# Performance work log

Measured on AMD Instinct MI355X. Metric: run time of the kernel, lower is better.

The kernel has to match this reference:

```python
import jax, jax.numpy as jnp
import numpy as np

E, D, O, G, H, K = 8, 1024, 1024, 512, 2048, 2
B = 8192

def _xavier(key, shape):
    fan_in, fan_out = shape[-2], shape[-1]
    lim = float(np.sqrt(6.0 / (fan_in + fan_out)))
    return jax.random.uniform(key, shape, jnp.float32, -lim, lim)

def setup_inputs() -> dict:
    key = jax.random.key(0)
    ks = jax.random.split(key, 6)
    x = jax.random.normal(ks[0], (B, D), jnp.float32)
    # stacked expert params (xavier-uniform weights, zero bias like torch init)
    W1 = _xavier(ks[1], (E, D, H))
    b1 = jnp.zeros((E, H), jnp.float32)
    W2 = _xavier(ks[2], (E, H, O))
    b2 = jnp.zeros((E, O), jnp.float32)
    # gate params
    Wg1 = _xavier(ks[3], (D, G))
    bg1 = jnp.zeros((G,), jnp.float32)
    Wg2 = _xavier(ks[4], (G, E))
    bg2 = jnp.zeros((E,), jnp.float32)
    return {"x": x, "W1": W1, "b1": b1, "W2": W2, "b2": b2,
            "Wg1": Wg1, "bg1": bg1, "Wg2": Wg2, "bg2": bg2}

def reference(x, W1, b1, W2, b2, Wg1, bg1, Wg2, bg2):
    batch = x.shape[0]
    # gate (dropout inactive in eval)
    gate_logits = jax.nn.relu(x @ Wg1 + bg1) @ Wg2 + bg2          # [B,E]
    gate_scores = jax.nn.softmax(gate_logits, axis=1)
    top_k_scores, top_k_indices = jax.lax.top_k(gate_scores, K)   # [B,K]
    # dense all-expert MLP (mirrors torch.stack over experts)
    h = jax.nn.relu(jnp.einsum('bd,edh->ebh', x, W1) + b1[:, None, :])   # [E,B,H]
    expert_outputs = jnp.einsum('ebh,eho->beo', h, W2) + b2[None, :, :]  # [B,E,O]
    # gather top-k expert outputs, scale, combine
    selected = jnp.take_along_axis(expert_outputs, top_k_indices[:, :, None], axis=1)  # [B,K,O]
    scaled = selected * top_k_scores[:, :, None]
    scaled = scaled / (jnp.sum(top_k_scores, axis=1, keepdims=True)[:, :, None] + 1e-9)
    combined = jnp.sum(scaled, axis=1)                            # [B,O]
    # auxiliary loss
    one_hot = jax.nn.one_hot(top_k_indices, E, dtype=jnp.float32) # [B,K,E]
    expert_load = jnp.sum(one_hot, axis=(0, 1)) / (batch + 1e-9)
    load_balancing_loss = jnp.var(expert_load, ddof=1)            # torch var is unbiased
    entropy = -jnp.mean(jnp.sum(gate_scores * jnp.log(gate_scores + 1e-9), axis=1))
    aux_loss = load_balancing_loss + entropy
    return combined, aux_loss
```

## Files before the change

### kernel.cpp

```cpp
#include <hip/hip_runtime.h>

#define B_ 8192
#define D_ 1024
#define O_ 1024
#define G_ 512
#define H_ 2048
#define E_ 8
#define ROWSP (B_ * 2 + E_ * 128)
#define TAU 0.01f

typedef unsigned short u16;
using f32x4 = __attribute__((ext_vector_type(4))) float;
using s16x8 = __attribute__((ext_vector_type(8))) short;

__device__ __forceinline__ u16 f2bf(float f) {
  union { float f; unsigned u; } v; v.f = f;
  unsigned r = v.u + 0x7FFFu + ((v.u >> 16) & 1u);
  return (u16)(r >> 16);
}
__device__ __forceinline__ float bf2f(u16 h) {
  union { unsigned u; float f; } v; v.u = ((unsigned)h) << 16; return v.f;
}
__device__ __forceinline__ void gload16(const void* g, void* l) {
  __builtin_amdgcn_global_load_lds(
      (const __attribute__((address_space(1))) unsigned int*)g,
      (__attribute__((address_space(3))) unsigned int*)l, 16, 0, 0);
}
__device__ __forceinline__ int xcd_swz(int bid, int nwg) {
  return (bid & 7) * (nwg >> 3) + (bid >> 3);
}
__device__ __forceinline__ int stage_kc(int t) {
  return (((t & 3) ^ ((t >> 3) & 3)) * 8);
}
__device__ __forceinline__ int frag_idx(int half, int lane, int i) {
  int row = half * 64 + i * 16 + (lane & 15);
  int s = (lane >> 4) ^ ((lane >> 1) & 3);
  return (row * 4 + s) * 8;
}

__global__ __launch_bounds__(256) void k_cast_x(const float* __restrict__ x,
                                                u16* __restrict__ xhi,
                                                u16* __restrict__ xlo) {
  int t = blockIdx.x * 256 + threadIdx.x;
  float4 v = ((const float4*)x)[t];
  u16 h0 = f2bf(v.x), h1 = f2bf(v.y), h2 = f2bf(v.z), h3 = f2bf(v.w);
  ushort4 hi; hi.x = h0; hi.y = h1; hi.z = h2; hi.w = h3;
  ushort4 lo;
  lo.x = f2bf(v.x - bf2f(h0)); lo.y = f2bf(v.y - bf2f(h1));
  lo.z = f2bf(v.z - bf2f(h2)); lo.w = f2bf(v.w - bf2f(h3));
  ((ushort4*)xhi)[t] = hi; ((ushort4*)xlo)[t] = lo;
}

__global__ __launch_bounds__(256) void k_transpose_cast(const float* __restrict__ src,
                                                        u16* __restrict__ dhi,
                                                        u16* __restrict__ dlo,
                                                        int R, int C) {
  __shared__ float tile[32][33];
  size_t bofs = (size_t)blockIdx.z * R * C;
  src += bofs; dhi += bofs; if (dlo) dlo += bofs;
  int tx = threadIdx.x & 31, ty = threadIdx.x >> 5;
  int c0 = blockIdx.x * 32, r0 = blockIdx.y * 32;
#pragma unroll
  for (int p = 0; p < 4; ++p) {
    int r = ty + p * 8;
    tile[r][tx] = src[(size_t)(r0 + r) * C + c0 + tx];
  }
  __syncthreads();
#pragma unroll
  for (int p = 0; p < 4; ++p) {
    int r = ty + p * 8;
    float v = tile[tx][r];
    size_t o = (size_t)(c0 + r) * R + r0 + tx;
    dhi[o] = f2bf(v);
    if (dlo) dlo[o] = f2bf(v - bf2f(f2bf(v)));
  }
}

__global__ __launch_bounds__(256) void k_gate_gemm1(const u16* __restrict__ xhi,
                                                    const u16* __restrict__ xlo,
                                                    const u16* __restrict__ whi,
                                                    const u16* __restrict__ wlo,
                                                    const float* __restrict__ bg1,
                                                    float* __restrict__ G1) {
  __shared__ u16 Ah[4096], Al[4096], Bh[4096], Bl[4096];
  int work = xcd_swz(blockIdx.x, (G_ / 128) * (B_ / 128));
  int m0 = (work >> 2) * 128, n0 = (work & 3) * 128;
  int t = threadIdx.x;
  int wave = t >> 6, lane = t & 63;
  int wm = wave >> 1, wn = wave & 1;

  const f32x4 z = {0.f, 0.f, 0.f, 0.f};
  f32x4 acc[4][4];
#pragma unroll
  for (int i = 0; i < 4; ++i)
#pragma unroll
    for (int j = 0; j < 4; ++j) acc[i][j] = z;

  int ar = t >> 2, ac = stage_kc(t);
  const u16* xh0 = xhi + (size_t)(m0 + ar) * D_ + ac;
  const u16* xh1 = xhi + (size_t)(m0 + 64 + ar) * D_ + ac;
  const u16* xl0 = xlo + (size_t)(m0 + ar) * D_ + ac;
  const u16* xl1 = xlo + (size_t)(m0 + 64 + ar) * D_ + ac;
  const u16* wh0 = whi + (size_t)(n0 + ar) * D_ + ac;
  const u16* wh1 = whi + (size_t)(n0 + 64 + ar) * D_ + ac;
  const u16* wl0 = wlo + (size_t)(n0 + ar) * D_ + ac;
  const u16* wl1 = wlo + (size_t)(n0 + 64 + ar) * D_ + ac;

  for (int k0 = 0; k0 < D_; k0 += 32) {
    gload16(xh0 + k0, &Ah[t * 8]); gload16(xh1 + k0, &Ah[2048 + t * 8]);
    gload16(xl0 + k0, &Al[t * 8]); gload16(xl1 + k0, &Al[2048 + t * 8]);
    gload16(wh0 + k0, &Bh[t * 8]); gload16(wh1 + k0, &Bh[2048 + t * 8]);
    gload16(wl0 + k0, &Bl[t * 8]); gload16(wl1 + k0, &Bl[2048 + t * 8]);
    __syncthreads();
    s16x8 ah[4], al[4], bh[4], bl[4];
#pragma unroll
    for (int i = 0; i < 4; ++i) {
      ah[i] = *(const s16x8*)&Ah[frag_idx(wm, lane, i)];
      al[i] = *(const s16x8*)&Al[frag_idx(wm, lane, i)];
      bh[i] = *(const s16x8*)&Bh[frag_idx(wn, lane, i)];
      bl[i] = *(const s16x8*)&Bl[frag_idx(wn, lane, i)];
    }
#pragma unroll
    for (int i = 0; i < 4; ++i)
#pragma unroll
      for (int j = 0; j < 4; ++j) {
        acc[i][j] = __builtin_amdgcn_mfma_f32_16x16x32_bf16(ah[i], bh[j], acc[i][j], 0, 0, 0);
        acc[i][j] = __builtin_amdgcn_mfma_f32_16x16x32_bf16(ah[i], bl[j], acc[i][j], 0, 0, 0);
        acc[i][j] = __builtin_amdgcn_mfma_f32_16x16x32_bf16(al[i], bh[j], acc[i][j], 0, 0, 0);
      }
    __syncthreads();
  }
#pragma unroll
  for (int j = 0; j < 4; ++j) {
    int col = n0 + wn * 64 + j * 16 + (lane & 15);
    float bias = bg1[col];
#pragma unroll
    for (int i = 0; i < 4; ++i)
#pragma unroll
      for (int q = 0; q < 4; ++q) {
        int row = m0 + wm * 64 + i * 16 + (lane >> 4) * 4 + q;
        float v = acc[i][j][q] + bias;
        G1[(size_t)row * G_ + col] = v > 0.f ? v : 0.f;
      }
  }
}

__global__ __launch_bounds__(256) void k_gate_logits(const float* __restrict__ G1,
                                                     const float* __restrict__ Wg2,
                                                     const float* __restrict__ bg2,
                                                     float* __restrict__ logits,
                                                     int* __restrict__ flaglist,
                                                     int* __restrict__ nflag) {
  int t = threadIdx.x, wave = t >> 6, lane = t & 63;
  int row = blockIdx.x * 4 + wave;

  float4 g0 = *(const float4*)(G1 + (size_t)row * G_ + lane * 8);
  float4 g1 = *(const float4*)(G1 + (size_t)row * G_ + lane * 8 + 4);
  float g[8] = {g0.x, g0.y, g0.z, g0.w, g1.x, g1.y, g1.z, g1.w};
  float p[8] = {0, 0, 0, 0, 0, 0, 0, 0};
#pragma unroll
  for (int cc = 0; cc < 8; ++cc) {
    int c = lane * 8 + cc;
    float4 w0 = *(const float4*)(Wg2 + c * 8);
    float4 w1 = *(const float4*)(Wg2 + c * 8 + 4);
    p[0] += g[cc] * w0.x; p[1] += g[cc] * w0.y; p[2] += g[cc] * w0.z; p[3] += g[cc] * w0.w;
    p[4] += g[cc] * w1.x; p[5] += g[cc] * w1.y; p[6] += g[cc] * w1.z; p[7] += g[cc] * w1.w;
  }
#pragma unroll
  for (int off = 32; off >= 1; off >>= 1)
#pragma unroll
    for (int e = 0; e < 8; ++e) p[e] += __shfl_xor(p[e], off);
  if (lane == 0) {
    float l1 = -1e30f, l2 = -1e30f, l3 = -1e30f;
#pragma unroll
    for (int e = 0; e < 8; ++e) {
      float v = p[e] + bg2[e];
      logits[(size_t)row * 8 + e] = v;
      if (v > l1) { l3 = l2; l2 = l1; l1 = v; }
      else if (v > l2) { l3 = l2; l2 = v; }
      else if (v > l3) { l3 = v; }
    }
    if (l2 - l3 < TAU) {
      int pos = atomicAdd(nflag, 1);
      flaglist[pos] = row;
    }
  }
}

__global__ __launch_bounds__(256) void k_gate_fixup(const float* __restrict__ x,
                                                    const float* __restrict__ Wg1,
                                                    const float* __restrict__ bg1,
                                                    const float* __restrict__ Wg2,
                                                    const float* __restrict__ bg2,
                                                    const int* __restrict__ flaglist,
                                                    const int* __restrict__ nflag,
                                                    float* __restrict__ logits) {
  __shared__ float xs[1024];
  __shared__ float red[256][9];
  int t = threadIdx.x;
  int n = *nflag;
  for (int i = blockIdx.x; i < n; i += gridDim.x) {
    int row = flaglist[i];
    ((float4*)xs)[t] = ((const float4*)(x + (size_t)row * D_))[t];
    __syncthreads();
    int c0 = t * 2;
    float h0 = 0.f, h1 = 0.f;
#pragma unroll 8
    for (int d = 0; d < D_; ++d) {
      float xv = xs[d];
      float2 w = *(const float2*)(Wg1 + (size_t)d * G_ + c0);
      h0 += xv * w.x; h1 += xv * w.y;
    }
    h0 += bg1[c0]; h1 += bg1[c0 + 1];
    h0 = h0 > 0.f ? h0 : 0.f; h1 = h1 > 0.f ? h1 : 0.f;
#pragma unroll
    for (int e = 0; e < 8; ++e)
      red[t][e] = h0 * Wg2[c0 * 8 + e] + h1 * Wg2[(c0 + 1) * 8 + e];
    __syncthreads();
    for (int s = 128; s >= 1; s >>= 1) {
      if (t < s) {
#pragma unroll
        for (int e = 0; e < 8; ++e) red[t][e] += red[t + s][e];
      }
      __syncthreads();
    }
    if (t < 8) logits[(size_t)row * 8 + t] = red[0][t] + bg2[t];
    __syncthreads();
  }
}

__global__ __launch_bounds__(256) void k_gate_final(const float* __restrict__ logits,
                                                    int* __restrict__ topidx,
                                                    float* __restrict__ wnorm,
                                                    int* __restrict__ counts,
                                                    float* __restrict__ entacc) {
  __shared__ int cnt_s[8];
  __shared__ float ent_s[4];
  int t = threadIdx.x;
  if (t < 8) cnt_s[t] = 0;
  __syncthreads();
  int row = blockIdx.x * 256 + t;
  float4 a = ((const float4*)logits)[(size_t)row * 2];
  float4 b = ((const float4*)logits)[(size_t)row * 2 + 1];
  float L[8] = {a.x, a.y, a.z, a.w, b.x, b.y, b.z, b.w};
  float m = L[0];
#pragma unroll
  for (int e = 1; e < 8; ++e) m = fmaxf(m, L[e]);
  float s[8], Z = 0.f;
#pragma unroll
  for (int e = 0; e < 8; ++e) { s[e] = expf(L[e] - m); Z += s[e]; }
  float inv = 1.f / Z;
  float sc[8];
#pragma unroll
  for (int e = 0; e < 8; ++e) sc[e] = s[e] * inv;
  int i1 = 0;
#pragma unroll
  for (int e = 1; e < 8; ++e) if (L[e] > L[i1]) i1 = e;
  int i2 = (i1 == 0) ? 1 : 0;
#pragma unroll
  for (int e = 0; e < 8; ++e) if (e != i1 && L[e] > L[i2]) i2 = e;
  float s1 = sc[i1], s2 = sc[i2];
  float denom = s1 + s2 + 1e-9f;
  topidx[row * 2] = i1; topidx[row * 2 + 1] = i2;
  wnorm[row * 2] = s1 / denom; wnorm[row * 2 + 1] = s2 / denom;
  atomicAdd(&cnt_s[i1], 1); atomicAdd(&cnt_s[i2], 1);
  float ent = 0.f;
#pragma unroll
  for (int e = 0; e < 8; ++e) ent -= sc[e] * logf(sc[e] + 1e-9f);
#pragma unroll
  for (int off = 32; off >= 1; off >>= 1) ent += __shfl_xor(ent, off);
  if ((t & 63) == 0) ent_s[t >> 6] = ent;
  __syncthreads();
  if (t == 0) atomicAdd(entacc, ent_s[0] + ent_s[1] + ent_s[2] + ent_s[3]);
  if (t < 8) atomicAdd(&counts[t], cnt_s[t]);
}

__global__ void k_scan(const int* __restrict__ counts, const float* __restrict__ entacc,
                       int* __restrict__ aoff, float* __restrict__ aux_out) {
  if (threadIdx.x == 0 && blockIdx.x == 0) {
    int off = 0; aoff[0] = 0;
    float ld[8]; float mean = 0.f;
    for (int e = 0; e < 8; ++e) {
      ld[e] = (float)counts[e] / (8192.0f + 1e-9f);
      mean += ld[e];
      off += ((counts[e] + 127) >> 7) << 7;
      aoff[e + 1] = off;
    }
    mean *= 0.125f;
    float var = 0.f;
    for (int e = 0; e < 8; ++e) { float d = ld[e] - mean; var += d * d; }
    var *= (1.0f / 7.0f);
    *aux_out = var + entacc[0] / 8192.0f;
  }
}

__global__ __launch_bounds__(256) void k_scatter(const int* __restrict__ topidx,
                                                 const float* __restrict__ wnorm,
                                                 const int* __restrict__ aoff,
                                                 int* __restrict__ fill,
                                                 int* __restrict__ tok_list,
                                                 float* __restrict__ wroute,
                                                 int* __restrict__ pos_of) {
  int t = blockIdx.x * 256 + threadIdx.x;
  if (t >= B_ * 2) return;
  int e = topidx[t];
  int pos = aoff[e] + atomicAdd(&fill[e], 1);
  tok_list[pos] = t >> 1;
  wroute[pos] = wnorm[t];
  pos_of[t] = pos;
}

__global__ __launch_bounds__(256) void k_egemm1(const u16* __restrict__ xhi,
                                                const u16* __restrict__ w1t,
                                                const float* __restrict__ b1v,
                                                const int* __restrict__ tok_list,
                                                const int* __restrict__ aoff,
                                                u16* __restrict__ hbuf) {
  __shared__ u16 As[2][4096], Bs[2][4096];
  int work = xcd_swz(blockIdx.x, (H_ / 128) * (ROWSP / 128));
  int rt = work >> 4;
  int n0 = (work & 15) * 128;
  int row0 = rt * 128;
  if (row0 >= aoff[8]) return;
  int e = 0;
  while (row0 >= aoff[e + 1]) ++e;
  int t = threadIdx.x, wave = t >> 6, lane = t & 63;
  int wm = wave >> 1, wn = wave & 1;
  const u16* w1e = w1t + (size_t)e * H_ * D_;

  int ar = t >> 2, ac = stage_kc(t);
  int tok0 = tok_list[row0 + ar];       if ((unsigned)tok0 >= B_) tok0 = 0;
  int tok1 = tok_list[row0 + 64 + ar];  if ((unsigned)tok1 >= B_) tok1 = 0;
  const u16* a0 = xhi + (size_t)tok0 * D_ + ac;
  const u16* a1 = xhi + (size_t)tok1 * D_ + ac;
  const u16* bb0 = w1e + (size_t)(n0 + ar) * D_ + ac;
  const u16* bb1 = w1e + (size_t)(n0 + 64 + ar) * D_ + ac;

  const f32x4 z = {0.f, 0.f, 0.f, 0.f};
  f32x4 acc[4][4];
#pragma unroll
  for (int i = 0; i < 4; ++i)
#pragma unroll
    for (int j = 0; j < 4; ++j) acc[i][j] = z;

  gload16(a0, &As[0][t * 8]);  gload16(a1, &As[0][2048 + t * 8]);
  gload16(bb0, &Bs[0][t * 8]); gload16(bb1, &Bs[0][2048 + t * 8]);
  __syncthreads();

  const int NT = D_ / 32;
  for (int kt = 0; kt < NT; ++kt) {
    const u16* Sa = As[kt & 1];
    const u16* Sb = Bs[kt & 1];
    if (kt + 1 < NT) {
      int k1 = (kt + 1) * 32;
      u16* Da = As[(kt + 1) & 1];
      u16* Db = Bs[(kt + 1) & 1];
      gload16(a0 + k1, &Da[t * 8]);  gload16(a1 + k1, &Da[2048 + t * 8]);
      gload16(bb0 + k1, &Db[t * 8]); gload16(bb1 + k1, &Db[2048 + t * 8]);
    }
    s16x8 af[4], bf[4];
#pragma unroll
    for (int i = 0; i < 4; ++i) {
      af[i] = *(const s16x8*)&Sa[frag_idx(wm, lane, i)];
      bf[i] = *(const s16x8*)&Sb[frag_idx(wn, lane, i)];
    }
#pragma unroll
    for (int i = 0; i < 4; ++i)
#pragma unroll
      for (int j = 0; j < 4; ++j)
        acc[i][j] = __builtin_amdgcn_mfma_f32_16x16x32_bf16(af[i], bf[j], acc[i][j], 0, 0, 0);
    __syncthreads();
  }
#pragma unroll
  for (int j = 0; j < 4; ++j) {
    int col = n0 + wn * 64 + j * 16 + (lane & 15);
    float bias = b1v[e * H_ + col];
#pragma unroll
    for (int i = 0; i < 4; ++i)
#pragma unroll
      for (int q = 0; q < 4; ++q) {
        int row = row0 + wm * 64 + i * 16 + (lane >> 4) * 4 + q;
        float v = acc[i][j][q] + bias;
        hbuf[(size_t)row * H_ + col] = f2bf(v > 0.f ? v : 0.f);
      }
  }
}

__global__ __launch_bounds__(256) void k_egemm2(const u16* __restrict__ hbuf,
                                                const u16* __restrict__ w2t,
                                                const float* __restrict__ b2v,
                                                const int* __restrict__ aoff,
                                                const float* __restrict__ wroute,
                                                u16* __restrict__ rbuf) {
  __shared__ u16 As[2][4096], Bs[2][4096];
  int work = xcd_swz(blockIdx.x, (O_ / 128) * (ROWSP / 128));
  int rt = work >> 3;
  int n0 = (work & 7) * 128;
  int row0 = rt * 128;
  if (row0 >= aoff[8]) return;
  int e = 0;
  while (row0 >= aoff[e + 1]) ++e;
  int t = threadIdx.x, wave = t >> 6, lane = t & 63;
  int wm = wave >> 1, wn = wave & 1;
  const u16* w2e = w2t + (size_t)e * O_ * H_;

  int ar = t >> 2, ac = stage_kc(t);
  const u16* a0 = hbuf + (size_t)(row0 + ar) * H_ + ac;
  const u16* a1 = hbuf + (size_t)(row0 + 64 + ar) * H_ + ac;
  const u16* bb0 = w2e + (size_t)(n0 + ar) * H_ + ac;
  const u16* bb1 = w2e + (size_t)(n0 + 64 + ar) * H_ + ac;

  const f32x4 z = {0.f, 0.f, 0.f, 0.f};
  f32x4 acc[4][4];
#pragma unroll
  for (int i = 0; i < 4; ++i)
#pragma unroll
    for (int j = 0; j < 4; ++j) acc[i][j] = z;

  gload16(a0, &As[0][t * 8]);  gload16(a1, &As[0][2048 + t * 8]);
  gload16(bb0, &Bs[0][t * 8]); gload16(bb1, &Bs[0][2048 + t * 8]);
  __syncthreads();

  const int NT = H_ / 32;
  for (int kt = 0; kt < NT; ++kt) {
    const u16* Sa = As[kt & 1];
    const u16* Sb = Bs[kt & 1];
    if (kt + 1 < NT) {
      int k1 = (kt + 1) * 32;
      u16* Da = As[(kt + 1) & 1];
      u16* Db = Bs[(kt + 1) & 1];
      gload16(a0 + k1, &Da[t * 8]);  gload16(a1 + k1, &Da[2048 + t * 8]);
      gload16(bb0 + k1, &Db[t * 8]); gload16(bb1 + k1, &Db[2048 + t * 8]);
    }
    s16x8 af[4], bf[4];
#pragma unroll
    for (int i = 0; i < 4; ++i) {
      af[i] = *(const s16x8*)&Sa[frag_idx(wm, lane, i)];
      bf[i] = *(const s16x8*)&Sb[frag_idx(wn, lane, i)];
    }
#pragma unroll
    for (int i = 0; i < 4; ++i)
#pragma unroll
      for (int j = 0; j < 4; ++j)
        acc[i][j] = __builtin_amdgcn_mfma_f32_16x16x32_bf16(af[i], bf[j], acc[i][j], 0, 0, 0);
    __syncthreads();
  }
#pragma unroll
  for (int i = 0; i < 4; ++i)
#pragma unroll
    for (int q = 0; q < 4; ++q) {
      int row = row0 + wm * 64 + i * 16 + (lane >> 4) * 4 + q;
      float wv = wroute[row];
#pragma unroll
      for (int j = 0; j < 4; ++j) {
        int col = n0 + wn * 64 + j * 16 + (lane & 15);
        float bias = b2v[e * O_ + col];
        rbuf[(size_t)row * O_ + col] = f2bf((acc[i][j][q] + bias) * wv);
      }
    }
}

__global__ __launch_bounds__(256) void k_combine(const u16* __restrict__ rbuf,
                                                 const int* __restrict__ pos_of,
                                                 float* __restrict__ out) {
  int t = threadIdx.x;
  int tok = blockIdx.x * 2 + (t >> 7);
  int c = (t & 127) * 8;
  int p0 = pos_of[tok * 2], p1 = pos_of[tok * 2 + 1];
  const u16* r0 = rbuf + (size_t)p0 * O_ + c;
  const u16* r1 = rbuf + (size_t)p1 * O_ + c;
  ushort4 a0 = *(const ushort4*)r0, a1 = *(const ushort4*)(r0 + 4);
  ushort4 b0 = *(const ushort4*)r1, b1 = *(const ushort4*)(r1 + 4);
  float4 o0, o1;
  o0.x = bf2f(a0.x) + bf2f(b0.x); o0.y = bf2f(a0.y) + bf2f(b0.y);
  o0.z = bf2f(a0.z) + bf2f(b0.z); o0.w = bf2f(a0.w) + bf2f(b0.w);
  o1.x = bf2f(a1.x) + bf2f(b1.x); o1.y = bf2f(a1.y) + bf2f(b1.y);
  o1.z = bf2f(a1.z) + bf2f(b1.z); o1.w = bf2f(a1.w) + bf2f(b1.w);
  float* op = out + (size_t)tok * O_ + c;
  *(float4*)op = o0; *(float4*)(op + 4) = o1;
}

static const size_t o_xhi  = 0;
static const size_t o_xlo  = o_xhi + (size_t)B_ * D_ * 2;
static const size_t o_w1t  = o_xlo + (size_t)B_ * D_ * 2;
static const size_t o_w2t  = o_w1t + (size_t)E_ * H_ * D_ * 2;
static const size_t o_wg1h = o_w2t + (size_t)E_ * O_ * H_ * 2;
static const size_t o_wg1l = o_wg1h + (size_t)G_ * D_ * 2;
static const size_t o_G1   = o_wg1l + (size_t)G_ * D_ * 2;
static const size_t o_h    = o_G1 + (size_t)B_ * G_ * 4;
static const size_t o_idx  = o_h + (size_t)ROWSP * H_ * 2;
static const size_t o_wn   = o_idx + (size_t)B_ * 2 * 4;
static const size_t o_pos  = o_wn + (size_t)B_ * 2 * 4;
static const size_t o_tok  = o_pos + (size_t)B_ * 2 * 4;
static const size_t o_wr   = o_tok + (size_t)ROWSP * 4;
static const size_t o_cnt  = o_wr + (size_t)ROWSP * 4;
static const size_t o_fill = o_cnt + 32;
static const size_t o_ent  = o_cnt + 64;
static const size_t o_nfl  = o_cnt + 96;
static const size_t o_aoff = o_cnt + 128;
static const size_t o_logits = o_cnt + 256;
static const size_t o_flag   = o_logits + (size_t)B_ * 8 * 4;
static const size_t o_rbuf = o_xlo;

extern "C" void kernel_launch(void* const* d_in, const int* in_sizes, int n_in,
                              void* d_out, int out_size, void* d_ws, size_t ws_size,
                              hipStream_t stream) {
  const float* x   = (const float*)d_in[0];
  const float* W1  = (const float*)d_in[1];
  const float* b1  = (const float*)d_in[2];
  const float* W2  = (const float*)d_in[3];
  const float* b2  = (const float*)d_in[4];
  const float* Wg1 = (const float*)d_in[5];
  const float* bg1 = (const float*)d_in[6];
  const float* Wg2 = (const float*)d_in[7];
  const float* bg2 = (const float*)d_in[8];
  float* out = (float*)d_out;
  char* ws = (char*)d_ws;

  u16* xhi  = (u16*)(ws + o_xhi);
  u16* xlo  = (u16*)(ws + o_xlo);
  u16* w1t  = (u16*)(ws + o_w1t);
  u16* w2t  = (u16*)(ws + o_w2t);
  u16* wg1h = (u16*)(ws + o_wg1h);
  u16* wg1l = (u16*)(ws + o_wg1l);
  float* G1 = (float*)(ws + o_G1);
  u16* hbuf = (u16*)(ws + o_h);
  int* topidx = (int*)(ws + o_idx);
  float* wnorm = (float*)(ws + o_wn);
  int* pos_of = (int*)(ws + o_pos);
  int* tok_list = (int*)(ws + o_tok);
  float* wroute = (float*)(ws + o_wr);
  int* counts = (int*)(ws + o_cnt);
  int* fill = (int*)(ws + o_fill);
  float* entacc = (float*)(ws + o_ent);
  int* nflag = (int*)(ws + o_nfl);
  int* aoff = (int*)(ws + o_aoff);
  float* logits = (float*)(ws + o_logits);
  int* flaglist = (int*)(ws + o_flag);
  u16* rbuf = (u16*)(ws + o_rbuf);

  hipMemsetAsync(ws + o_cnt, 0, 128, stream);

  k_cast_x<<<(B_ * D_ / 4) / 256, 256, 0, stream>>>(x, xhi, xlo);
  k_transpose_cast<<<dim3(G_ / 32, D_ / 32, 1), 256, 0, stream>>>(Wg1, wg1h, wg1l, D_, G_);
  k_transpose_cast<<<dim3(H_ / 32, D_ / 32, E_), 256, 0, stream>>>(W1, w1t, nullptr, D_, H_);
  k_transpose_cast<<<dim3(O_ / 32, H_ / 32, E_), 256, 0, stream>>>(W2, w2t, nullptr, H_, O_);

  k_gate_gemm1<<<(G_ / 128) * (B_ / 128), 256, 0, stream>>>(xhi, xlo, wg1h, wg1l, bg1, G1);
  k_gate_logits<<<B_ / 4, 256, 0, stream>>>(G1, Wg2, bg2, logits, flaglist, nflag);
  k_gate_fixup<<<128, 256, 0, stream>>>(x, Wg1, bg1, Wg2, bg2, flaglist, nflag, logits);
  k_gate_final<<<B_ / 256, 256, 0, stream>>>(logits, topidx, wnorm, counts, entacc);
  k_scan<<<1, 64, 0, stream>>>(counts, entacc, aoff, out + (size_t)B_ * O_);
  k_scatter<<<(B_ * 2) / 256, 256, 0, stream>>>(topidx, wnorm, aoff, fill, tok_list, wroute, pos_of);

  k_egemm1<<<(H_ / 128) * (ROWSP / 128), 256, 0, stream>>>(xhi, w1t, b1, tok_list, aoff, hbuf);
  k_egemm2<<<(O_ / 128) * (ROWSP / 128), 256, 0, stream>>>(hbuf, w2t, b2, aoff, wroute, rbuf);
  k_combine<<<B_ / 2, 256, 0, stream>>>(rbuf, pos_of, out);
}
```

Baseline: 514.7 us.

## Triple-buffer expert GEMM LDS tiles with explicit vmcnt waits

Both expert GEMM kernels move from a double-buffered to a three-stage LDS pipeline. Loads run two k-tiles ahead, and waits use explicit s_waitcnt vmcnt counts with raw s_barrier instead of __syncthreads. The aim is to hide global-to-LDS latency behind the MFMA work. In exchange, LDS use grows from 32KB to 48KB per block, which may reduce occupancy. The hand-counted vmcnt values must match the number of outstanding loads, or the kernels will read stale tiles.

```diff
diff --git a/kernel.cpp b/kernel.cpp
--- a/kernel.cpp
+++ b/kernel.cpp
@@ -316,7 +316,7 @@
                                                 const int* __restrict__ tok_list,
                                                 const int* __restrict__ aoff,
                                                 u16* __restrict__ hbuf) {
-  __shared__ u16 As[2][4096], Bs[2][4096];
+  __shared__ u16 As[3][4096], Bs[3][4096];
   int work = xcd_swz(blockIdx.x, (H_ / 128) * (ROWSP / 128));
   int rt = work >> 4;
   int n0 = (work & 15) * 128;
@@ -343,21 +343,22 @@
 #pragma unroll
     for (int j = 0; j < 4; ++j) acc[i][j] = z;
 
-  gload16(a0, &As[0][t * 8]);  gload16(a1, &As[0][2048 + t * 8]);
-  gload16(bb0, &Bs[0][t * 8]); gload16(bb1, &Bs[0][2048 + t * 8]);
-  __syncthreads();
+#pragma unroll
+  for (int s = 0; s < 3; ++s) {
+    int kk = s * 32;
+    gload16(a0 + kk, &As[s][t * 8]);  gload16(a1 + kk, &As[s][2048 + t * 8]);
+    gload16(bb0 + kk, &Bs[s][t * 8]); gload16(bb1 + kk, &Bs[s][2048 + t * 8]);
+  }
 
   const int NT = D_ / 32;
+  int cb = 0;
   for (int kt = 0; kt < NT; ++kt) {
-    const u16* Sa = As[kt & 1];
-    const u16* Sb = Bs[kt & 1];
-    if (kt + 1 < NT) {
-      int k1 = (kt + 1) * 32;
-      u16* Da = As[(kt + 1) & 1];
-      u16* Db = Bs[(kt + 1) & 1];
-      gload16(a0 + k1, &Da[t * 8]);  gload16(a1 + k1, &Da[2048 + t * 8]);
-      gload16(bb0 + k1, &Db[t * 8]); gload16(bb1 + k1, &Db[2048 + t * 8]);
-    }
+    if (kt < NT - 2)      asm volatile("s_waitcnt vmcnt(8)" ::: "memory");
+    else if (kt == NT - 2) asm volatile("s_waitcnt vmcnt(4)" ::: "memory");
+    else                  asm volatile("s_waitcnt vmcnt(0)" ::: "memory");
+    __builtin_amdgcn_s_barrier();
+    const u16* Sa = As[cb];
+    const u16* Sb = Bs[cb];
     s16x8 af[4], bf[4];
 #pragma unroll
     for (int i = 0; i < 4; ++i) {
@@ -369,7 +370,13 @@
 #pragma unroll
       for (int j = 0; j < 4; ++j)
         acc[i][j] = __builtin_amdgcn_mfma_f32_16x16x32_bf16(af[i], bf[j], acc[i][j], 0, 0, 0);
-    __syncthreads();
+    __builtin_amdgcn_s_barrier();
+    if (kt + 3 < NT) {
+      int kk = (kt + 3) * 32;
+      gload16(a0 + kk, &As[cb][t * 8]);  gload16(a1 + kk, &As[cb][2048 + t * 8]);
+      gload16(bb0 + kk, &Bs[cb][t * 8]); gload16(bb1 + kk, &Bs[cb][2048 + t * 8]);
+    }
+    cb = (cb == 2) ? 0 : cb + 1;
   }
 #pragma unroll
   for (int j = 0; j < 4; ++j) {
@@ -392,7 +399,7 @@
                                                 const int* __restrict__ aoff,
                                                 const float* __restrict__ wroute,
                                                 u16* __restrict__ rbuf) {
-  __shared__ u16 As[2][4096], Bs[2][4096];
+  __shared__ u16 As[3][4096], Bs[3][4096];
   int work = xcd_swz(blockIdx.x, (O_ / 128) * (ROWSP / 128));
   int rt = work >> 3;
   int n0 = (work & 7) * 128;
@@ -417,21 +424,22 @@
 #pragma unroll
     for (int j = 0; j < 4; ++j) acc[i][j] = z;
 
-  gload16(a0, &As[0][t * 8]);  gload16(a1, &As[0][2048 + t * 8]);
-  gload16(bb0, &Bs[0][t * 8]); gload16(bb1, &Bs[0][2048 + t * 8]);
-  __syncthreads();
+#pragma unroll
+  for (int s = 0; s < 3; ++s) {
+    int kk = s * 32;
+    gload16(a0 + kk, &As[s][t * 8]);  gload16(a1 + kk, &As[s][2048 + t * 8]);
+    gload16(bb0 + kk, &Bs[s][t * 8]); gload16(bb1 + kk, &Bs[s][2048 + t * 8]);
+  }
 
   const int NT = H_ / 32;
+  int cb = 0;
   for (int kt = 0; kt < NT; ++kt) {
-    const u16* Sa = As[kt & 1];
-    const u16* Sb = Bs[kt & 1];
-    if (kt + 1 < NT) {
-      int k1 = (kt + 1) * 32;
-      u16* Da = As[(kt + 1) & 1];
-      u16* Db = Bs[(kt + 1) & 1];
-      gload16(a0 + k1, &Da[t * 8]);  gload16(a1 + k1, &Da[2048 + t * 8]);
-      gload16(bb0 + k1, &Db[t * 8]); gload16(bb1 + k1, &Db[2048 + t * 8]);
-    }
+    if (kt < NT - 2)      asm volatile("s_waitcnt vmcnt(8)" ::: "memory");
+    else if (kt == NT - 2) asm volatile("s_waitcnt vmcnt(4)" ::: "memory");
+    else                  asm volatile("s_waitcnt vmcnt(0)" ::: "memory");
+    __builtin_amdgcn_s_barrier();
+    const u16* Sa = As[cb];
+    const u16* Sb = Bs[cb];
     s16x8 af[4], bf[4];
 #pragma unroll
     for (int i = 0; i < 4; ++i) {
@@ -443,7 +451,13 @@
 #pragma unroll
       for (int j = 0; j < 4; ++j)
         acc[i][j] = __builtin_amdgcn_mfma_f32_16x16x32_bf16(af[i], bf[j], acc[i][j], 0, 0, 0);
-    __syncthreads();
+    __builtin_amdgcn_s_barrier();
+    if (kt + 3 < NT) {
+      int kk = (kt + 3) * 32;
+      gload16(a0 + kk, &As[cb][t * 8]);  gload16(a1 + kk, &As[cb][2048 + t * 8]);
+      gload16(bb0 + kk, &Bs[cb][t * 8]); gload16(bb1 + kk, &Bs[cb][2048 + t * 8]);
+    }
+    cb = (cb == 2) ? 0 : cb + 1;
   }
 #pragma unroll
   for (int i = 0; i < 4; ++i)
```

New measurement: 520.7 us. About the same (+1.2%).
